# Kernel optimization log

Measured on AMD Instinct MI355X. Metric: run time of the kernel, lower is better.

## Reference

```python
import jax, jax.numpy as jnp
import numpy as np

PI = np.pi
NQ = 9  # qubits: edge 0-2, node 3-6 (center=3, neighbor0=4), anc1=7, anc2=8


def _mlp(x, W1, b1, W2, b2):
    h = jax.nn.leaky_relu(x @ W1 + b1, negative_slope=0.2)
    return h @ W2 + b2


def _ry(t):
    h = 0.5 * t
    c = jnp.cos(h).astype(jnp.complex64)
    s = jnp.sin(h).astype(jnp.complex64)
    return jnp.stack([jnp.stack([c, -s]), jnp.stack([s, c])])


def _rx(t):
    h = 0.5 * t
    c = jnp.cos(h).astype(jnp.complex64)
    s = jnp.sin(h).astype(jnp.complex64)
    return jnp.stack([jnp.stack([c, -1j * s]), jnp.stack([-1j * s, c])])


def _rz(t):
    h = (0.5 * t).astype(jnp.complex64)
    e = jnp.exp(-1j * h)
    z = jnp.zeros((), jnp.complex64)
    return jnp.stack([jnp.stack([e, z]), jnp.stack([z, jnp.conj(e)])])


def _ap1(state, U, q):
    s = jnp.moveaxis(state, q, 0)
    s = jnp.tensordot(U, s, axes=([1], [0]))
    return jnp.moveaxis(s, 0, q)


def _apc(state, U, c, t):  # controlled-U, control c, target t
    s = jnp.moveaxis(state, (c, t), (0, 1))
    s1 = jnp.tensordot(U, s[1], axes=([1], [0]))
    s = jnp.stack([s[0], s1])
    return jnp.moveaxis(s, (0, 1), (c, t))


def _cz(state, a, b):
    s = jnp.moveaxis(state, (a, b), (0, 1))
    s = s.at[1, 1].multiply(-1.0)
    return jnp.moveaxis(s, (0, 1), (a, b))


def _pqc(data, theta):
    # data: [18] per-graphlet angles, theta: [27] shared weights; returns <X_center>
    state = jnp.zeros((2,) * NQ, jnp.complex64).at[(0,) * NQ].set(1.0)
    for i in range(3):  # edge qubits: ry, rz
        state = _ap1(state, _ry(data[2 * i]), i)
        state = _ap1(state, _rz(data[2 * i + 1]), i)
    for i in range(4):  # node qubits: ry, rz
        state = _ap1(state, _ry(data[6 + 2 * i]), 3 + i)
        state = _ap1(state, _rz(data[7 + 2 * i]), 3 + i)
    state = _apc(state, _rx(data[14]), 4, 7)  # neighbor -> anc1, c-rx(phi0)
    state = _apc(state, _ry(data[15]), 0, 7)  # edge0    -> anc1, c-ry(phi1)
    state = _apc(state, _rz(data[16]), 4, 8)  # neighbor -> anc2, c-rz(phi2)
    state = _apc(state, _ry(data[17]), 0, 8)  # edge0    -> anc2, c-ry(phi3)
    for b, qs in enumerate([(0, 4, 7), (7, 4, 8), (3, 7, 8)]):  # A, B, U blocks
        th = theta[9 * b:9 * b + 9]
        for i, q in enumerate(qs):
            state = _ap1(state, _rx(th[3 * i + 0]), q)
            state = _ap1(state, _ry(th[3 * i + 1]), q)
            state = _ap1(state, _rz(th[3 * i + 2]), q)
        state = _cz(state, qs[0], qs[1])
        state = _cz(state, qs[1], qs[2])
        state = _cz(state, qs[2], qs[0])
    xs = jnp.moveaxis(jnp.moveaxis(state, 3, 0)[::-1], 0, 3)  # apply X on qubit 3
    return jnp.real(jnp.vdot(state, xs)).astype(jnp.float32)


def setup_inputs() -> dict:
    N, E, K, G = 6000, 96000, 4, 32
    rng = np.random.default_rng(0)
    src = rng.integers(0, N, E)
    dst = (src + 1 + rng.integers(0, N - 1, E)) % N  # no self loops
    pairs = np.stack([np.minimum(src, dst), np.maximum(src, dst)], 1)
    keymap = {(int(u), int(v)): i for i, (u, v) in enumerate(pairs)}
    und = np.unique(np.concatenate([np.stack([src, dst], 1), np.stack([dst, src], 1)], 0), axis=0)
    deg = np.bincount(und[:, 0], minlength=N)
    starts = np.concatenate([[0], np.cumsum(deg)])[:-1]
    gn = np.full((N, K), -1, np.int32)
    gn[:, 0] = np.arange(N)
    ge = np.full((N, K - 1), -1, np.int32)
    for j in range(K - 1):
        has = deg > j
        cs = np.nonzero(has)[0]
        nb = und[starts[has] + j, 1]
        gn[cs, 1 + j] = nb
        for c, n in zip(cs.tolist(), nb.tolist()):
            ge[c, j] = keymap[(min(c, n), max(c, n))]
    batch = ((np.arange(N) * G) // N).astype(np.int32)
    key = jax.random.key(0)
    ks = jax.random.split(key, 12)

    def dense(k, i, o):
        return jax.random.normal(k, (i, o), jnp.float32) / np.sqrt(i)

    return dict(
        node_feat=jax.random.normal(ks[0], (N, 16), jnp.float32),
        edge_attr=jax.random.normal(ks[1], (E, 8), jnp.float32),
        node_W1=dense(ks[2], 16, 128), node_b1=jnp.zeros((128,), jnp.float32),
        node_W2=dense(ks[3], 128, 2), node_b2=jnp.zeros((2,), jnp.float32),
        edge_W1=dense(ks[4], 8, 128), edge_b1=jnp.zeros((128,), jnp.float32),
        edge_W2=dense(ks[5], 128, 2), edge_b2=jnp.zeros((2,), jnp.float32),
        theta=jax.random.uniform(ks[6], (1, 27), jnp.float32, -0.1, 0.1),
        upd_W1=dense(ks[7], 3, 128)[None], upd_b1=jnp.zeros((1, 128), jnp.float32),
        upd_W2=dense(ks[8], 128, 2)[None], upd_b2=jnp.zeros((1, 2), jnp.float32),
        head_W1=dense(ks[9], 2, 2), head_b1=jnp.zeros((2,), jnp.float32),
        head_W2=dense(ks[10], 2, 2), head_b2=jnp.zeros((2,), jnp.float32),
        graphlet_nodes=jnp.asarray(gn), graphlet_edges=jnp.asarray(ge),
        batch=jnp.asarray(batch), num_graphs=G,
    )


def reference(node_feat, edge_attr, node_W1, node_b1, node_W2, node_b2,
              edge_W1, edge_b1, edge_W2, edge_b2, theta,
              upd_W1, upd_b1, upd_W2, upd_b2,
              head_W1, head_b1, head_W2, head_b2,
              graphlet_nodes, graphlet_edges, batch, num_graphs):
    node_f = jnp.tanh(_mlp(node_feat, node_W1, node_b1, node_W2, node_b2)) * PI
    edge_f = jnp.tanh(_mlp(edge_attr, edge_W1, edge_b1, edge_W2, edge_b2)) * PI
    nm = (graphlet_nodes >= 0).astype(node_f.dtype)[..., None]  # pad mask
    em = (graphlet_edges >= 0).astype(edge_f.dtype)[..., None]
    gn = jnp.clip(graphlet_nodes, 0)
    ge = jnp.clip(graphlet_edges, 0)
    N = node_f.shape[0]
    e_feat = edge_f[ge] * em  # [N,3,2] fixed across hops
    for h in range(theta.shape[0]):
        n_feat = node_f[gn] * nm  # [N,4,2]
        phis = jnp.stack([n_feat[:, 1, 0], e_feat[:, 0, 0], n_feat[:, 1, 1], e_feat[:, 0, 1]], 1)
        data = jnp.concatenate([e_feat.reshape(N, 6), n_feat.reshape(N, 8), phis], 1)  # [N,18]
        exp = jax.vmap(_pqc, in_axes=(0, None))(data, theta[h])  # [N]
        upd_inp = jnp.concatenate([node_f[gn[:, 0]], exp[:, None]], 1)  # [N,3]
        upd = _mlp(upd_inp, upd_W1[h], upd_b1[h], upd_W2[h], upd_b2[h])  # [N,2]
        node_f = node_f + jnp.zeros_like(node_f).at[gn[:, 0]].add(upd)
    seg = jax.ops.segment_sum(node_f, batch, num_segments=num_graphs)
    cnt = jax.ops.segment_sum(jnp.ones((N,), node_f.dtype), batch, num_segments=num_graphs)
    emb = seg / cnt[:, None]  # global mean pool
    return _mlp(emb, head_W1, head_b1, head_W2, head_b2)
```

## Files before the change

### kernel.cpp

```cpp
#include <hip/hip_runtime.h>

#define PI_F 3.14159265358979323846f

struct C2 { float r, i; };
struct M2 { C2 m[2][2]; };

__device__ __forceinline__ C2 cmul(C2 a, C2 b){ return C2{a.r*b.r - a.i*b.i, a.r*b.i + a.i*b.r}; }
__device__ __forceinline__ C2 cadd(C2 a, C2 b){ return C2{a.r+b.r, a.i+b.i}; }

__device__ __forceinline__ M2 mmul(M2 A, M2 B){
  M2 R;
  #pragma unroll
  for (int r=0;r<2;++r)
    #pragma unroll
    for (int c=0;c<2;++c)
      R.m[r][c] = cadd(cmul(A.m[r][0],B.m[0][c]), cmul(A.m[r][1],B.m[1][c]));
  return R;
}
__device__ __forceinline__ M2 m_rz(float t){ float s,c; __sincosf(0.5f*t,&s,&c);
  M2 U; U.m[0][0]=C2{c,-s}; U.m[0][1]=C2{0,0}; U.m[1][0]=C2{0,0}; U.m[1][1]=C2{c,s}; return U; }
__device__ __forceinline__ M2 m_ry(float t){ float s,c; __sincosf(0.5f*t,&s,&c);
  M2 U; U.m[0][0]=C2{c,0}; U.m[0][1]=C2{-s,0}; U.m[1][0]=C2{s,0}; U.m[1][1]=C2{c,0}; return U; }
__device__ __forceinline__ M2 m_rx(float t){ float s,c; __sincosf(0.5f*t,&s,&c);
  M2 U; U.m[0][0]=C2{c,0}; U.m[0][1]=C2{0,-s}; U.m[1][0]=C2{0,-s}; U.m[1][1]=C2{c,0}; return U; }
__device__ __forceinline__ M2 fuse_zyx(float tz, float ty, float tx){ return mmul(m_rz(tz), mmul(m_ry(ty), m_rx(tx))); }

__device__ __forceinline__ float fast_tanh(float x){
  float e = __expf(2.f*x);
  return 1.f - 2.f/(e + 1.f);
}

__device__ __forceinline__ M2 loadM(const float* __restrict__ p){
  M2 U;
  U.m[0][0]=C2{p[0],p[1]}; U.m[0][1]=C2{p[2],p[3]};
  U.m[1][0]=C2{p[4],p[5]}; U.m[1][1]=C2{p[6],p[7]};
  return U;
}


template<int T>
__device__ __forceinline__ void applyT(M2 U, float (&sr)[32], float (&si)[32]){
  #pragma unroll
  for (int a0=0;a0<32;++a0){
    if (a0 & T) continue;
    const int a1 = a0 | T;
    C2 x0{sr[a0], si[a0]}, x1{sr[a1], si[a1]};
    C2 n0 = cadd(cmul(U.m[0][0],x0), cmul(U.m[0][1],x1));
    C2 n1 = cadd(cmul(U.m[1][0],x0), cmul(U.m[1][1],x1));
    sr[a0]=n0.r; si[a0]=n0.i; sr[a1]=n1.r; si[a1]=n1.i;
  }
}

template<int BA,int BB,int BC>
__device__ __forceinline__ void czTriple(float (&sr)[32], float (&si)[32]){
  #pragma unroll
  for (int a=0;a<32;++a){
    const int x=(a&BA)?1:0, y=(a&BB)?1:0, z=(a&BC)?1:0;
    if (((x&y)^(y&z)^(z&x)) != 0){ sr[a]=-sr[a]; si[a]=-si[a]; }
  }
}

__global__ void features_kernel(const float* __restrict__ node_feat,
                                const float* __restrict__ edge_attr,
                                const int* __restrict__ ge,
                                const float* __restrict__ nW1, const float* __restrict__ nb1,
                                const float* __restrict__ nW2, const float* __restrict__ nb2,
                                const float* __restrict__ eW1, const float* __restrict__ eb1,
                                const float* __restrict__ eW2, const float* __restrict__ eb2,
                                float* __restrict__ node_f, float* __restrict__ ef,
                                int N,
                                const float* __restrict__ theta, float* __restrict__ tm){
  const int row = blockIdx.x*blockDim.x + threadIdx.x;
  if (row < 9){
    M2 U = fuse_zyx(theta[3*row+2], theta[3*row+1], theta[3*row+0]);
    float* p = tm + row*8;
    p[0]=U.m[0][0].r; p[1]=U.m[0][0].i;
    p[2]=U.m[0][1].r; p[3]=U.m[0][1].i;
    p[4]=U.m[1][0].r; p[5]=U.m[1][0].i;
    p[6]=U.m[1][1].r; p[7]=U.m[1][1].i;
  }
  if (row < N){
    float xi[16];
    #pragma unroll
    for (int i=0;i<16;++i) xi[i] = node_feat[row*16+i];
    float a0 = nb2[0], a1 = nb2[1];
    #pragma unroll 4
    for (int j=0;j<128;++j){
      float h = nb1[j];
      #pragma unroll
      for (int i=0;i<16;++i) h = fmaf(xi[i], nW1[i*128+j], h);
      h = h > 0.f ? h : 0.2f*h;
      a0 = fmaf(h, nW2[j*2+0], a0);
      a1 = fmaf(h, nW2[j*2+1], a1);
    }
    node_f[row*2+0] = PI_F * fast_tanh(a0);
    node_f[row*2+1] = PI_F * fast_tanh(a1);
  } else {
    const int r = row - N;
    if (r >= N) return;
    const int e = ge[r*3+0];
    if (e < 0){ ef[r*2+0] = 0.f; ef[r*2+1] = 0.f; return; }
    float xi[8];
    #pragma unroll
    for (int i=0;i<8;++i) xi[i] = edge_attr[e*8+i];
    float a0 = eb2[0], a1 = eb2[1];
    #pragma unroll 4
    for (int j=0;j<128;++j){
      float h = eb1[j];
      #pragma unroll
      for (int i=0;i<8;++i) h = fmaf(xi[i], eW1[i*128+j], h);
      h = h > 0.f ? h : 0.2f*h;
      a0 = fmaf(h, eW2[j*2+0], a0);
      a1 = fmaf(h, eW2[j*2+1], a1);
    }
    ef[r*2+0] = PI_F * fast_tanh(a0);
    ef[r*2+1] = PI_F * fast_tanh(a1);
  }
}

__global__ void __launch_bounds__(64, 1)
pqc_kernel(const float* __restrict__ node_f, const float* __restrict__ ef,
           const int* __restrict__ gn,
           const float* __restrict__ tm,
           const float* __restrict__ uW1, const float* __restrict__ ub1,
           const float* __restrict__ uW2, const float* __restrict__ ub2,
           float* __restrict__ upd, int N){
  const int n = blockIdx.x*64 + threadIdx.x;
  if (n >= N) return;

  const float e0 = ef[n*2+0], e1 = ef[n*2+1];
  const float f0 = node_f[n*2+0], f1 = node_f[n*2+1];
  const int v1 = gn[n*4+1];
  const bool ok = v1 >= 0; const int idx = ok ? v1 : 0;
  const float g0 = ok ? node_f[idx*2+0] : 0.f;
  const float g1 = ok ? node_f[idx*2+1] : 0.f;

  float sy0,cy0,sz0,cz0, sy3,cy3,sz3,cz3, sy4,cy4,sz4,cz4;
  __sincosf(0.5f*e0,&sy0,&cy0); __sincosf(0.5f*e1,&sz0,&cz0);
  __sincosf(0.5f*f0,&sy3,&cy3); __sincosf(0.5f*f1,&sz3,&cz3);
  __sincosf(0.5f*g0,&sy4,&cy4); __sincosf(0.5f*g1,&sz4,&cz4);

  const C2 v0[2] = { C2{cy0*cz0, -cy0*sz0}, C2{sy0*cz0, sy0*sz0} };
  const C2 v3[2] = { C2{cy3*cz3, -cy3*sz3}, C2{sy3*cz3, sy3*sz3} };
  const C2 v4[2] = { C2{cy4*cz4, -cy4*sz4}, C2{sy4*cz4, sy4*sz4} };

  float sr[32], si[32];
  #pragma unroll
  for (int a=0;a<32;++a){ sr[a]=0.f; si[a]=0.f; }
  #pragma unroll
  for (int b4=0;b4<2;++b4){
    #pragma unroll
    for (int b3=0;b3<2;++b3){
      const C2 t = cmul(v0[b4], v3[b3]);
      #pragma unroll
      for (int b2=0;b2<2;++b2){
        const C2 a = cmul(t, v4[b2]);
        const int ix = b4*16 + b3*8 + b2*4;
        sr[ix]=a.r; si[ix]=a.i;
      }
    }
  }

  #pragma unroll
  for (int a0=0;a0<32;++a0){
    if ((a0 & 2) || !(a0 & 4)) continue;
    const int a1 = a0 | 2;
    const float r0=sr[a0], i0=si[a0], r1=sr[a1], i1=si[a1];
    sr[a0] = cy4*r0 + sy4*i1;  si[a0] = cy4*i0 - sy4*r1;
    sr[a1] = sy4*i0 + cy4*r1;  si[a1] = -sy4*r0 + cy4*i1;
  }
  #pragma unroll
  for (int a0=0;a0<32;++a0){
    if ((a0 & 2) || !(a0 & 16)) continue;
    const int a1 = a0 | 2;
    const float r0=sr[a0], i0=si[a0], r1=sr[a1], i1=si[a1];
    sr[a0] = cy0*r0 - sy0*r1;  si[a0] = cy0*i0 - sy0*i1;
    sr[a1] = sy0*r0 + cy0*r1;  si[a1] = sy0*i0 + cy0*i1;
  }
  #pragma unroll
  for (int a=0;a<32;++a){
    if (!(a & 4)) continue;
    const float r=sr[a], im=si[a];
    if (a & 1){ sr[a] = r*cz4 - im*sz4;  si[a] = im*cz4 + r*sz4; }
    else      { sr[a] = r*cz4 + im*sz4;  si[a] = im*cz4 - r*sz4; }
  }
  #pragma unroll
  for (int a0=0;a0<32;++a0){
    if ((a0 & 1) || !(a0 & 16)) continue;
    const int a1 = a0 | 1;
    const float r0=sr[a0], i0=si[a0], r1=sr[a1], i1=si[a1];
    sr[a0] = cz0*r0 - sz0*r1;  si[a0] = cz0*i0 - sz0*i1;
    sr[a1] = sz0*r0 + cz0*r1;  si[a1] = sz0*i0 + cz0*i1;
  }

  applyT<16>(loadM(tm+0*8), sr, si);
  applyT< 4>(loadM(tm+1*8), sr, si);
  applyT< 2>(loadM(tm+2*8), sr, si);
  czTriple<16,4,2>(sr, si);
  applyT< 2>(loadM(tm+3*8), sr, si);
  applyT< 4>(loadM(tm+4*8), sr, si);
  applyT< 1>(loadM(tm+5*8), sr, si);
  czTriple<2,4,1>(sr, si);
  applyT< 8>(loadM(tm+6*8), sr, si);
  applyT< 2>(loadM(tm+7*8), sr, si);
  applyT< 1>(loadM(tm+8*8), sr, si);
  czTriple<8,2,1>(sr, si);

  float acc = 0.f;
  #pragma unroll
  for (int a=0;a<32;++a) acc += sr[a]*sr[a^8] + si[a]*si[a^8];

  float o0 = ub2[0], o1 = ub2[1];
  #pragma unroll 4
  for (int j=0;j<128;++j){
    float h = ub1[j];
    h = fmaf(f0,  uW1[0*128+j], h);
    h = fmaf(f1,  uW1[1*128+j], h);
    h = fmaf(acc, uW1[2*128+j], h);
    h = h > 0.f ? h : 0.2f*h;
    o0 = fmaf(h, uW2[j*2+0], o0);
    o1 = fmaf(h, uW2[j*2+1], o1);
  }
  upd[n*2+0] = o0;
  upd[n*2+1] = o1;
}

__global__ void reduce_head_kernel(const float* __restrict__ node_f,
                                   const float* __restrict__ upd,
                                   const float* __restrict__ hW1, const float* __restrict__ hb1,
                                   const float* __restrict__ hW2, const float* __restrict__ hb2,
                                   float* __restrict__ out, int N, int G){
  const int g = blockIdx.x;
  const int start = (g*N + G - 1)/G;
  const int end   = ((g+1)*N + G - 1)/G;
  float a0=0.f, a1=0.f;
  for (int n = start + threadIdx.x; n < end; n += 64){
    a0 += node_f[n*2+0] + upd[n*2+0];
    a1 += node_f[n*2+1] + upd[n*2+1];
  }
  #pragma unroll
  for (int m=32; m; m>>=1){ a0 += __shfl_xor(a0, m); a1 += __shfl_xor(a1, m); }
  if (threadIdx.x == 0){
    const float inv = 1.f / (float)(end - start);
    const float e0 = a0*inv, e1 = a1*inv;
    float h0 = hb1[0] + e0*hW1[0*2+0] + e1*hW1[1*2+0];
    float h1 = hb1[1] + e0*hW1[0*2+1] + e1*hW1[1*2+1];
    h0 = h0 > 0.f ? h0 : 0.2f*h0;
    h1 = h1 > 0.f ? h1 : 0.2f*h1;
    out[g*2+0] = hb2[0] + h0*hW2[0*2+0] + h1*hW2[1*2+0];
    out[g*2+1] = hb2[1] + h0*hW2[0*2+1] + h1*hW2[1*2+1];
  }
}

extern "C" void kernel_launch(void* const* d_in, const int* in_sizes, int n_in,
                              void* d_out, int out_size, void* d_ws, size_t ws_size,
                              hipStream_t stream) {
  const float* node_feat = (const float*)d_in[0];
  const float* edge_attr = (const float*)d_in[1];
  const float* nW1 = (const float*)d_in[2];
  const float* nb1 = (const float*)d_in[3];
  const float* nW2 = (const float*)d_in[4];
  const float* nb2 = (const float*)d_in[5];
  const float* eW1 = (const float*)d_in[6];
  const float* eb1 = (const float*)d_in[7];
  const float* eW2 = (const float*)d_in[8];
  const float* eb2 = (const float*)d_in[9];
  const float* theta = (const float*)d_in[10];
  const float* uW1 = (const float*)d_in[11];
  const float* ub1 = (const float*)d_in[12];
  const float* uW2 = (const float*)d_in[13];
  const float* ub2 = (const float*)d_in[14];
  const float* hW1 = (const float*)d_in[15];
  const float* hb1 = (const float*)d_in[16];
  const float* hW2 = (const float*)d_in[17];
  const float* hb2 = (const float*)d_in[18];
  const int* gn    = (const int*)d_in[19];
  const int* ge    = (const int*)d_in[20];

  const int N = in_sizes[0] / 16;
  const int G = out_size / 2;

  float* node_f = (float*)d_ws;
  float* ef     = node_f + (size_t)N*2;
  float* upd    = ef + (size_t)N*2;
  float* tm     = upd + (size_t)N*2;

  const int R = 2*N;
  features_kernel<<<(R+255)/256, 256, 0, stream>>>(node_feat, edge_attr, ge,
                                                   nW1, nb1, nW2, nb2,
                                                   eW1, eb1, eW2, eb2,
                                                   node_f, ef, N, theta, tm);
  pqc_kernel<<<(N+63)/64, 64, 0, stream>>>(node_f, ef, gn, tm,
                                           uW1, ub1, uW2, ub2, upd, N);
  reduce_head_kernel<<<G, 64, 0, stream>>>(node_f, upd,
                                           hW1, hb1, hW2, hb2, (float*)d_out, N, G);
}
```

Before: 136.2 us.

## Split PQC statevector across thread pairs along edge-qubit axis

Each graphlet's 32-amplitude statevector is now split across two lanes by the edge0 qubit, so each thread holds 16 amplitudes. Gates on that qubit use lane shuffles, and its controlled gates become per-lane conditional rotations. The update MLP's hidden loop is also split between the two lanes and combined with shuffles. The residual add moves into the PQC kernel, and the feature loads are vectorised to float4. This halves per-thread register use and doubles thread count to raise occupancy, at the cost of shuffle traffic and some duplicated setup work.

```diff
diff --git a/kernel.cpp b/kernel.cpp
--- a/kernel.cpp
+++ b/kernel.cpp
@@ -39,9 +39,9 @@
 
 
 template<int T>
-__device__ __forceinline__ void applyT(M2 U, float (&sr)[32], float (&si)[32]){
-  #pragma unroll
-  for (int a0=0;a0<32;++a0){
+__device__ __forceinline__ void applyT16(M2 U, float (&sr)[16], float (&si)[16]){
+  #pragma unroll
+  for (int a0=0;a0<16;++a0){
     if (a0 & T) continue;
     const int a1 = a0 | T;
     C2 x0{sr[a0], si[a0]}, x1{sr[a1], si[a1]};
@@ -51,10 +51,26 @@
   }
 }
 
+__device__ __forceinline__ void applyQ0(M2 U, int p, float (&sr)[16], float (&si)[16]){
+  const float u0r = p ? U.m[1][0].r : U.m[0][0].r;
+  const float u0i = p ? U.m[1][0].i : U.m[0][0].i;
+  const float u1r = p ? U.m[1][1].r : U.m[0][1].r;
+  const float u1i = p ? U.m[1][1].i : U.m[0][1].i;
+  #pragma unroll
+  for (int a=0;a<16;++a){
+    const float orr = __shfl_xor(sr[a], 1);
+    const float oii = __shfl_xor(si[a], 1);
+    const float xar = p ? orr   : sr[a], xai = p ? oii   : si[a];
+    const float xbr = p ? sr[a] : orr,   xbi = p ? si[a] : oii;
+    sr[a] = u0r*xar - u0i*xai + u1r*xbr - u1i*xbi;
+    si[a] = u0r*xai + u0i*xar + u1r*xbi + u1i*xbr;
+  }
+}
+
 template<int BA,int BB,int BC>
-__device__ __forceinline__ void czTriple(float (&sr)[32], float (&si)[32]){
-  #pragma unroll
-  for (int a=0;a<32;++a){
+__device__ __forceinline__ void czTriple16(float (&sr)[16], float (&si)[16]){
+  #pragma unroll
+  for (int a=0;a<16;++a){
     const int x=(a&BA)?1:0, y=(a&BB)?1:0, z=(a&BC)?1:0;
     if (((x&y)^(y&z)^(z&x)) != 0){ sr[a]=-sr[a]; si[a]=-si[a]; }
   }
@@ -80,9 +96,10 @@
     p[6]=U.m[1][1].r; p[7]=U.m[1][1].i;
   }
   if (row < N){
-    float xi[16];
-    #pragma unroll
-    for (int i=0;i<16;++i) xi[i] = node_feat[row*16+i];
+    const float4* nf4 = reinterpret_cast<const float4*>(node_feat + (size_t)row*16);
+    const float4 A = nf4[0], B = nf4[1], C = nf4[2], D = nf4[3];
+    const float xi[16] = {A.x,A.y,A.z,A.w, B.x,B.y,B.z,B.w,
+                          C.x,C.y,C.z,C.w, D.x,D.y,D.z,D.w};
     float a0 = nb2[0], a1 = nb2[1];
     #pragma unroll 4
     for (int j=0;j<128;++j){
@@ -100,9 +117,9 @@
     if (r >= N) return;
     const int e = ge[r*3+0];
     if (e < 0){ ef[r*2+0] = 0.f; ef[r*2+1] = 0.f; return; }
-    float xi[8];
-    #pragma unroll
-    for (int i=0;i<8;++i) xi[i] = edge_attr[e*8+i];
+    const float4* ea4 = reinterpret_cast<const float4*>(edge_attr + (size_t)e*8);
+    const float4 A = ea4[0], B = ea4[1];
+    const float xi[8] = {A.x,A.y,A.z,A.w, B.x,B.y,B.z,B.w};
     float a0 = eb2[0], a1 = eb2[1];
     #pragma unroll 4
     for (int j=0;j<128;++j){
@@ -125,7 +142,9 @@
            const float* __restrict__ uW1, const float* __restrict__ ub1,
            const float* __restrict__ uW2, const float* __restrict__ ub2,
            float* __restrict__ upd, int N){
-  const int n = blockIdx.x*64 + threadIdx.x;
+  const int t = blockIdx.x*64 + threadIdx.x;
+  const int n = t >> 1;
+  const int p = t & 1;
   if (n >= N) return;
 
   const float e0 = ef[n*2+0], e1 = ef[n*2+1];
@@ -143,76 +162,90 @@
   const C2 v0[2] = { C2{cy0*cz0, -cy0*sz0}, C2{sy0*cz0, sy0*sz0} };
   const C2 v3[2] = { C2{cy3*cz3, -cy3*sz3}, C2{sy3*cz3, sy3*sz3} };
   const C2 v4[2] = { C2{cy4*cz4, -cy4*sz4}, C2{sy4*cz4, sy4*sz4} };
-
-  float sr[32], si[32];
-  #pragma unroll
-  for (int a=0;a<32;++a){ sr[a]=0.f; si[a]=0.f; }
-  #pragma unroll
-  for (int b4=0;b4<2;++b4){
-    #pragma unroll
-    for (int b3=0;b3<2;++b3){
-      const C2 t = cmul(v0[b4], v3[b3]);
-      #pragma unroll
-      for (int b2=0;b2<2;++b2){
-        const C2 a = cmul(t, v4[b2]);
-        const int ix = b4*16 + b3*8 + b2*4;
-        sr[ix]=a.r; si[ix]=a.i;
-      }
-    }
-  }
-
-  #pragma unroll
-  for (int a0=0;a0<32;++a0){
+  const C2 v0p = p ? v0[1] : v0[0];
+
+  float sr[16], si[16];
+  #pragma unroll
+  for (int a=0;a<16;++a){ sr[a]=0.f; si[a]=0.f; }
+  #pragma unroll
+  for (int b3=0;b3<2;++b3){
+    const C2 tt = cmul(v0p, v3[b3]);
+    #pragma unroll
+    for (int b2=0;b2<2;++b2){
+      const C2 a = cmul(tt, v4[b2]);
+      const int ix = b3*8 + b2*4;
+      sr[ix]=a.r; si[ix]=a.i;
+    }
+  }
+
+  #pragma unroll
+  for (int a0=0;a0<16;++a0){
     if ((a0 & 2) || !(a0 & 4)) continue;
     const int a1 = a0 | 2;
     const float r0=sr[a0], i0=si[a0], r1=sr[a1], i1=si[a1];
     sr[a0] = cy4*r0 + sy4*i1;  si[a0] = cy4*i0 - sy4*r1;
     sr[a1] = sy4*i0 + cy4*r1;  si[a1] = -sy4*r0 + cy4*i1;
   }
-  #pragma unroll
-  for (int a0=0;a0<32;++a0){
-    if ((a0 & 2) || !(a0 & 16)) continue;
-    const int a1 = a0 | 2;
-    const float r0=sr[a0], i0=si[a0], r1=sr[a1], i1=si[a1];
-    sr[a0] = cy0*r0 - sy0*r1;  si[a0] = cy0*i0 - sy0*i1;
-    sr[a1] = sy0*r0 + cy0*r1;  si[a1] = sy0*i0 + cy0*i1;
-  }
-  #pragma unroll
-  for (int a=0;a<32;++a){
+  {
+    const float sA = p ? sy0 : 0.f, cA = p ? cy0 : 1.f;
+    #pragma unroll
+    for (int a0=0;a0<16;++a0){
+      if (a0 & 2) continue;
+      const int a1 = a0 | 2;
+      const float r0=sr[a0], i0=si[a0], r1=sr[a1], i1=si[a1];
+      sr[a0] = cA*r0 - sA*r1;  si[a0] = cA*i0 - sA*i1;
+      sr[a1] = sA*r0 + cA*r1;  si[a1] = sA*i0 + cA*i1;
+    }
+  }
+  #pragma unroll
+  for (int a=0;a<16;++a){
     if (!(a & 4)) continue;
     const float r=sr[a], im=si[a];
     if (a & 1){ sr[a] = r*cz4 - im*sz4;  si[a] = im*cz4 + r*sz4; }
     else      { sr[a] = r*cz4 + im*sz4;  si[a] = im*cz4 - r*sz4; }
   }
-  #pragma unroll
-  for (int a0=0;a0<32;++a0){
-    if ((a0 & 1) || !(a0 & 16)) continue;
-    const int a1 = a0 | 1;
-    const float r0=sr[a0], i0=si[a0], r1=sr[a1], i1=si[a1];
-    sr[a0] = cz0*r0 - sz0*r1;  si[a0] = cz0*i0 - sz0*i1;
-    sr[a1] = sz0*r0 + cz0*r1;  si[a1] = sz0*i0 + cz0*i1;
-  }
-
-  applyT<16>(loadM(tm+0*8), sr, si);
-  applyT< 4>(loadM(tm+1*8), sr, si);
-  applyT< 2>(loadM(tm+2*8), sr, si);
-  czTriple<16,4,2>(sr, si);
-  applyT< 2>(loadM(tm+3*8), sr, si);
-  applyT< 4>(loadM(tm+4*8), sr, si);
-  applyT< 1>(loadM(tm+5*8), sr, si);
-  czTriple<2,4,1>(sr, si);
-  applyT< 8>(loadM(tm+6*8), sr, si);
-  applyT< 2>(loadM(tm+7*8), sr, si);
-  applyT< 1>(loadM(tm+8*8), sr, si);
-  czTriple<8,2,1>(sr, si);
+  {
+    const float sB = p ? sz0 : 0.f, cB = p ? cz0 : 1.f;
+    #pragma unroll
+    for (int a0=0;a0<16;++a0){
+      if (a0 & 1) continue;
+      const int a1 = a0 | 1;
+      const float r0=sr[a0], i0=si[a0], r1=sr[a1], i1=si[a1];
+      sr[a0] = cB*r0 - sB*r1;  si[a0] = cB*i0 - sB*i1;
+      sr[a1] = sB*r0 + cB*r1;  si[a1] = sB*i0 + cB*i1;
+    }
+  }
+
+  applyQ0(loadM(tm+0*8), p, sr, si);
+  applyT16<4>(loadM(tm+1*8), sr, si);
+  applyT16<2>(loadM(tm+2*8), sr, si);
+  {
+    const float sg = p ? -1.f : 1.f;
+    #pragma unroll
+    for (int a=0;a<16;++a){
+      const int y=(a>>2)&1, z=(a>>1)&1;
+      if (y & z)      { sr[a]=-sr[a];  si[a]=-si[a]; }
+      else if (y | z) { sr[a]*=sg;     si[a]*=sg;    }
+    }
+  }
+  applyT16<2>(loadM(tm+3*8), sr, si);
+  applyT16<4>(loadM(tm+4*8), sr, si);
+  applyT16<1>(loadM(tm+5*8), sr, si);
+  czTriple16<2,4,1>(sr, si);
+  applyT16<8>(loadM(tm+6*8), sr, si);
+  applyT16<2>(loadM(tm+7*8), sr, si);
+  applyT16<1>(loadM(tm+8*8), sr, si);
+  czTriple16<8,2,1>(sr, si);
 
   float acc = 0.f;
   #pragma unroll
-  for (int a=0;a<32;++a) acc += sr[a]*sr[a^8] + si[a]*si[a^8];
-
-  float o0 = ub2[0], o1 = ub2[1];
+  for (int a=0;a<16;++a) acc += sr[a]*sr[a^8] + si[a]*si[a^8];
+  acc += __shfl_xor(acc, 1);
+
+  float o0 = 0.f, o1 = 0.f;
   #pragma unroll 4
-  for (int j=0;j<128;++j){
+  for (int jj=0;jj<64;++jj){
+    const int j = 2*jj + p;
     float h = ub1[j];
     h = fmaf(f0,  uW1[0*128+j], h);
     h = fmaf(f1,  uW1[1*128+j], h);
@@ -221,12 +254,15 @@
     o0 = fmaf(h, uW2[j*2+0], o0);
     o1 = fmaf(h, uW2[j*2+1], o1);
   }
-  upd[n*2+0] = o0;
-  upd[n*2+1] = o1;
-}
-
-__global__ void reduce_head_kernel(const float* __restrict__ node_f,
-                                   const float* __restrict__ upd,
+  o0 += __shfl_xor(o0, 1);
+  o1 += __shfl_xor(o1, 1);
+  if (!p){
+    *reinterpret_cast<float2*>(upd + (size_t)n*2) =
+        float2{f0 + ub2[0] + o0, f1 + ub2[1] + o1};
+  }
+}
+
+__global__ void reduce_head_kernel(const float* __restrict__ upd,
                                    const float* __restrict__ hW1, const float* __restrict__ hb1,
                                    const float* __restrict__ hW2, const float* __restrict__ hb2,
                                    float* __restrict__ out, int N, int G){
@@ -235,8 +271,9 @@
   const int end   = ((g+1)*N + G - 1)/G;
   float a0=0.f, a1=0.f;
   for (int n = start + threadIdx.x; n < end; n += 64){
-    a0 += node_f[n*2+0] + upd[n*2+0];
-    a1 += node_f[n*2+1] + upd[n*2+1];
+    const float2 u = *reinterpret_cast<const float2*>(upd + (size_t)n*2);
+    a0 += u.x;
+    a1 += u.y;
   }
   #pragma unroll
   for (int m=32; m; m>>=1){ a0 += __shfl_xor(a0, m); a1 += __shfl_xor(a1, m); }
@@ -290,8 +327,8 @@
                                                    nW1, nb1, nW2, nb2,
                                                    eW1, eb1, eW2, eb2,
                                                    node_f, ef, N, theta, tm);
-  pqc_kernel<<<(N+63)/64, 64, 0, stream>>>(node_f, ef, gn, tm,
-                                           uW1, ub1, uW2, ub2, upd, N);
-  reduce_head_kernel<<<G, 64, 0, stream>>>(node_f, upd,
+  pqc_kernel<<<(2*N+63)/64, 64, 0, stream>>>(node_f, ef, gn, tm,
+                                             uW1, ub1, uW2, ub2, upd, N);
+  reduce_head_kernel<<<G, 64, 0, stream>>>(upd,
                                            hW1, hb1, hW2, hb2, (float*)d_out, N, G);
 }
```

After: 133.4 us. -2.0%, faster.
